# Kernel optimization log

Measured on AMD Instinct MI355X. Metric: run time of the kernel, lower is better.

## Reference

```python
import jax, jax.numpy as jnp
import numpy as np

N = 8192
D_IN, D_HID, D_OUT = 64, 128, 64


def setup_inputs() -> dict:
    key = jax.random.key(0)
    ks = jax.random.split(key, 8)
    x = jax.random.normal(ks[0], (N, D_IN), dtype=jnp.float32)
    adj = jax.random.uniform(ks[1], (N, N), dtype=jnp.float32)
    s = 0.05  # small init scale
    W0 = jax.random.normal(ks[2], (D_IN, D_HID), dtype=jnp.float32) * s
    b0 = jnp.zeros((D_HID,), dtype=jnp.float32)
    W1 = jax.random.normal(ks[3], (D_HID, D_HID), dtype=jnp.float32) * s
    b1 = jnp.zeros((D_HID,), dtype=jnp.float32)
    W2 = jax.random.normal(ks[4], (D_HID, D_OUT), dtype=jnp.float32) * s
    b2 = jnp.zeros((D_OUT,), dtype=jnp.float32)
    return {"x": x, "adj": adj, "W0": W0, "b0": b0, "W1": W1, "b1": b1, "W2": W2, "b2": b2}


def laplacian_norm(adj):
    # A_hat = A + I; D^{-1/2} A_hat D^{-1/2}
    A = adj + jnp.eye(adj.shape[0], dtype=adj.dtype)
    dinv = jax.lax.rsqrt(jnp.sum(A, axis=1))
    return A * dinv[:, None] * dinv[None, :]


def reference(x, adj, W0, b0, W1, b1, W2, b2):
    An = laplacian_norm(adj)              # [N, N], computed once, reused per layer
    h = jax.nn.relu(An @ (x @ W0) + b0)   # layer 0 + hidden act
    h = jax.nn.relu(An @ (h @ W1) + b1)   # layer 1 + hidden act
    out = An @ (h @ W2) + b2              # last layer, identity out_act
    return out
```

## Files before the change

### kernel.cpp

```cpp
#include <hip/hip_runtime.h>
#include <type_traits>

typedef unsigned short u16;
typedef unsigned int   u32;
using short8 = __attribute__((ext_vector_type(8))) short;
using f32x4  = __attribute__((ext_vector_type(4))) float;

#define GLD_AS1 const __attribute__((address_space(1))) unsigned
#define GLD_AS3 __attribute__((address_space(3))) unsigned

static constexpr int NN = 8192;

__device__ __forceinline__ u16 f2bf(float f) {
  u32 u = __builtin_bit_cast(u32, f);
  u32 r = (u + 0x7FFFu + ((u >> 16) & 1u)) >> 16;
  return (u16)r;
}
__device__ __forceinline__ float bf2f(u16 h) {
  return __builtin_bit_cast(float, (u32)h << 16);
}
__device__ __forceinline__ short8 cvt8(f32x4 f0, f32x4 f1) {
  short8 r;
#pragma unroll
  for (int i = 0; i < 4; ++i) {
    r[i]     = (short)f2bf(f0[i]);
    r[4 + i] = (short)f2bf(f1[i]);
  }
  return r;
}

__global__ __launch_bounds__(256) void rowsum_cvt_k(const float* __restrict__ adj,
                                                    u16* __restrict__ adjb,
                                                    float* __restrict__ dinv) {
  const int row = blockIdx.x;
  const f32x4* p = (const f32x4*)(adj + (size_t)row * NN);
  short8* w = (short8*)(adjb + (size_t)row * NN);
  float s = 0.f;
#pragma unroll
  for (int i = 0; i < 4; ++i) {
    const int idx = threadIdx.x + i * 256;
    f32x4 v0 = __builtin_nontemporal_load(p + 2 * idx);
    f32x4 v1 = __builtin_nontemporal_load(p + 2 * idx + 1);
    s += (v0[0] + v0[1]) + (v0[2] + v0[3]) + (v1[0] + v1[1]) + (v1[2] + v1[3]);
    w[idx] = cvt8(v0, v1);
  }
#pragma unroll
  for (int off = 32; off > 0; off >>= 1) s += __shfl_down(s, off, 64);
  __shared__ float partial[4];
  if ((threadIdx.x & 63) == 0) partial[threadIdx.x >> 6] = s;
  __syncthreads();
  if (threadIdx.x == 0)
    dinv[row] = rsqrtf(partial[0] + partial[1] + partial[2] + partial[3] + 1.0f);
}

template <typename TIN>
__global__ __launch_bounds__(256) void featmul_k(const TIN* __restrict__ X,
                                                 const float* __restrict__ W,
                                                 const float* __restrict__ dinv,
                                                 u16* __restrict__ Gt,
                                                 u16* __restrict__ U,
                                                 int K, int C) {
  __shared__ __align__(16) u16 Wt[128][128];
  __shared__ float red[4][16][32];
  const int tid = threadIdx.x;
  for (int idx = tid; idx < 128 * 128; idx += 256) {
    int c = idx & 127, k = idx >> 7;
    float w = (k < K && c < C) ? W[k * C + c] : 0.f;
    Wt[c][k] = f2bf(w);
  }
  __syncthreads();
  const int wv = tid >> 6, lane = tid & 63;
  const int q = lane >> 4, m16 = lane & 15;
  const int r0 = blockIdx.x * 16;
  const int c0 = wv * 32;
  f32x4 acc[2];
  acc[0] = {0.f, 0.f, 0.f, 0.f};
  acc[1] = {0.f, 0.f, 0.f, 0.f};
  const TIN* xrow = X + (size_t)(r0 + m16) * K;
  for (int k = 0; k < K; k += 32) {
    short8 af;
    if constexpr (std::is_same_v<TIN, float>) {
      f32x4 f0 = *(const f32x4*)(xrow + k + q * 8);
      f32x4 f1 = *(const f32x4*)(xrow + k + q * 8 + 4);
      af = cvt8(f0, f1);
    } else {
      af = __builtin_bit_cast(short8, *(const uint4*)(xrow + k + q * 8));
    }
#pragma unroll
    for (int nh = 0; nh < 2; ++nh) {
      short8 bf = *(const short8*)&Wt[c0 + nh * 16 + m16][k + q * 8];
      acc[nh] = __builtin_amdgcn_mfma_f32_16x16x32_bf16(af, bf, acc[nh], 0, 0, 0);
    }
  }
#pragma unroll
  for (int nh = 0; nh < 2; ++nh)
#pragma unroll
    for (int reg = 0; reg < 4; ++reg)
      red[wv][q * 4 + reg][nh * 16 + m16] = acc[nh][reg];
  __syncthreads();
  {
    const int cc = lane & 31, rh = lane >> 5;
    short8 t;
#pragma unroll
    for (int i = 0; i < 8; ++i) {
      int r = rh * 8 + i;
      t[i] = (short)f2bf(red[wv][r][cc] * dinv[r0 + r]);
      U[(size_t)(r0 + r) * 128 + c0 + cc] = (u16)t[i];
    }
    *(uint4*)(Gt + (size_t)(c0 + cc) * NN + r0 + rh * 8) = __builtin_bit_cast(uint4, t);
  }
}

__global__ __launch_bounds__(512, 2) void gcn_gemm(const u16* __restrict__ Adjb,
                                                   const u16* __restrict__ Gt,
                                                   float* __restrict__ P) {
  __shared__ __align__(16) u16 As[3][256 * 64];
  __shared__ __align__(16) u16 Bs[3][128 * 64];

  const int tid = threadIdx.x;
  const int wv = tid >> 6, lane = tid & 63;
  const int wm = wv >> 1, wn = wv & 1;
  const int q = lane >> 4, m16 = lane & 15;
  const int mbase = blockIdx.x * 256;
  const int kbase = blockIdx.y * 1024;
  float* Pt = P + (size_t)blockIdx.y * NN * 128;

  size_t aoff[4];
  int acl[4];
  size_t boff[2];
  int bcl[2];
#pragma unroll
  for (int i = 0; i < 4; ++i) {
    const int cl = i * 512 + tid;
    const int r = cl >> 3;
    const int g = (cl & 7) ^ (r & 7);
    aoff[i] = (size_t)(mbase + r) * NN + g * 8;
    acl[i] = cl;
  }
#pragma unroll
  for (int i = 0; i < 2; ++i) {
    const int cl = i * 512 + tid;
    const int r = cl >> 3;
    const int g = (cl & 7) ^ (r & 7);
    boff[i] = (size_t)r * NN + g * 8;
    bcl[i] = cl;
  }

  auto stage = [&](int buf, int kc) {
#pragma unroll
    for (int i = 0; i < 4; ++i)
      __builtin_amdgcn_global_load_lds((GLD_AS1*)(Adjb + aoff[i] + kc),
                                       (GLD_AS3*)(&As[buf][acl[i] * 8]), 16, 0, 0);
#pragma unroll
    for (int i = 0; i < 2; ++i)
      __builtin_amdgcn_global_load_lds((GLD_AS1*)(Gt + boff[i] + kc),
                                       (GLD_AS3*)(&Bs[buf][bcl[i] * 8]), 16, 0, 0);
  };

  f32x4 acc[4][4];
#pragma unroll
  for (int a = 0; a < 4; ++a)
#pragma unroll
    for (int b = 0; b < 4; ++b) acc[a][b] = {0.f, 0.f, 0.f, 0.f};

  stage(0, kbase);
  stage(1, kbase + 64);
  for (int t = 0; t < 16; ++t) {
    const int buf = t % 3;
    if (t < 15) {
      asm volatile("s_waitcnt vmcnt(6)" ::: "memory");
    } else {
      asm volatile("s_waitcnt vmcnt(0)" ::: "memory");
    }
    __builtin_amdgcn_s_barrier();
    asm volatile("" ::: "memory");
    if (t + 2 < 16) stage((t + 2) % 3, kbase + (t + 2) * 64);
#pragma unroll
    for (int j = 0; j < 2; ++j) {
      short8 af[4], bf[4];
#pragma unroll
      for (int i = 0; i < 4; ++i) {
        const int m = wm * 64 + i * 16 + m16;
        const int n = wn * 64 + i * 16 + m16;
        af[i] = *(const short8*)&As[buf][m * 64 + (((j * 4 + q) ^ (m & 7)) << 3)];
        bf[i] = *(const short8*)&Bs[buf][n * 64 + (((j * 4 + q) ^ (n & 7)) << 3)];
      }
#pragma unroll
      for (int a = 0; a < 4; ++a)
#pragma unroll
        for (int b = 0; b < 4; ++b)
          acc[a][b] = __builtin_amdgcn_mfma_f32_16x16x32_bf16(af[a], bf[b], acc[a][b], 0, 0, 0);
    }
  }

#pragma unroll
  for (int a = 0; a < 4; ++a) {
#pragma unroll
    for (int b = 0; b < 4; ++b) {
      const int c = wn * 64 + b * 16 + m16;
#pragma unroll
      for (int reg = 0; reg < 4; ++reg) {
        const int r = mbase + wm * 64 + a * 16 + q * 4 + reg;
        Pt[(size_t)r * 128 + c] = acc[a][b][reg];
      }
    }
  }
}

template <int RELU, int OUT_F32>
__global__ __launch_bounds__(256) void finalize_k(const float* __restrict__ P,
                                                  const u16* __restrict__ U,
                                                  const float* __restrict__ dinv,
                                                  const float* __restrict__ bias,
                                                  u16* __restrict__ Hout,
                                                  float* __restrict__ Fout) {
  const int tid = threadIdx.x;
  const int c = tid & 127;
  const int r = blockIdx.x * 2 + (tid >> 7);
  const size_t idx = (size_t)r * 128 + c;
  float s = 0.f;
#pragma unroll
  for (int k = 0; k < 8; ++k) s += P[(size_t)k * NN * 128 + idx];
  s += bf2f(U[idx]);
  s = dinv[r] * s + bias[c];
  if (RELU) s = fmaxf(s, 0.f);
  if (OUT_F32) {
    if (c < 64) Fout[(size_t)r * 64 + c] = s;
  } else {
    Hout[idx] = f2bf(s);
  }
}

extern "C" void kernel_launch(void* const* d_in, const int* in_sizes, int n_in,
                              void* d_out, int out_size, void* d_ws, size_t ws_size,
                              hipStream_t stream) {
  const float* x   = (const float*)d_in[0];
  const float* adj = (const float*)d_in[1];
  const float* W0  = (const float*)d_in[2];
  const float* b0  = (const float*)d_in[3];
  const float* W1  = (const float*)d_in[4];
  const float* b1  = (const float*)d_in[5];
  const float* W2  = (const float*)d_in[6];
  const float* b2  = (const float*)d_in[7];
  float* out = (float*)d_out;

  char* ws = (char*)d_ws;
  float* dinv = (float*)ws;
  u16* Gt     = (u16*)(ws + (1u << 20));
  u16* U      = (u16*)(ws + (4u << 20));
  u16* h      = (u16*)(ws + (6u << 20));
  float* Pp   = (float*)(ws + (8u << 20));
  u16* adjb   = (u16*)(ws + (48u << 20));

  const dim3 ggrid(32, 8);

  rowsum_cvt_k<<<NN, 256, 0, stream>>>(adj, adjb, dinv);

  featmul_k<float><<<NN / 16, 256, 0, stream>>>(x, W0, dinv, Gt, U, 64, 128);
  gcn_gemm<<<ggrid, 512, 0, stream>>>(adjb, Gt, Pp);
  finalize_k<1, 0><<<NN / 2, 256, 0, stream>>>(Pp, U, dinv, b0, h, nullptr);

  featmul_k<u16><<<NN / 16, 256, 0, stream>>>(h, W1, dinv, Gt, U, 128, 128);
  gcn_gemm<<<ggrid, 512, 0, stream>>>(adjb, Gt, Pp);
  finalize_k<1, 0><<<NN / 2, 256, 0, stream>>>(Pp, U, dinv, b1, h, nullptr);

  featmul_k<u16><<<NN / 16, 256, 0, stream>>>(h, W2, dinv, Gt, U, 128, 64);
  gcn_gemm<<<ggrid, 512, 0, stream>>>(adjb, Gt, Pp);
  finalize_k<0, 1><<<NN / 2, 256, 0, stream>>>(Pp, U, dinv, b2, nullptr, out);
}
```

Baseline: 572.8 us.

## Replace direct global-to-LDS loads with register-staged double buffering and smaller tiles

The aggregation GEMM now uses 256-thread blocks on 128x128 output tiles, so the grid doubles in the M dimension. Tiles are prefetched two steps ahead into registers and written to a double-buffered LDS after compute, replacing the triple-buffered global_load_lds path. The aim is more blocks per CU and better overlap of loads with MFMA work. In exchange it uses more registers for staging, adds explicit LDS writes, and loads the G tile twice as many times because the M tile is smaller.

```diff
diff --git a/kernel.cpp b/kernel.cpp
--- a/kernel.cpp
+++ b/kernel.cpp
@@ -5,9 +5,6 @@
 typedef unsigned int   u32;
 using short8 = __attribute__((ext_vector_type(8))) short;
 using f32x4  = __attribute__((ext_vector_type(4))) float;
-
-#define GLD_AS1 const __attribute__((address_space(1))) unsigned
-#define GLD_AS3 __attribute__((address_space(3))) unsigned
 
 static constexpr int NN = 8192;
 
@@ -111,70 +108,61 @@
   }
 }
 
-__global__ __launch_bounds__(512, 2) void gcn_gemm(const u16* __restrict__ Adjb,
+__global__ __launch_bounds__(256, 2) void gcn_gemm(const u16* __restrict__ Adjb,
                                                    const u16* __restrict__ Gt,
                                                    float* __restrict__ P) {
-  __shared__ __align__(16) u16 As[3][256 * 64];
-  __shared__ __align__(16) u16 Bs[3][128 * 64];
+  __shared__ __align__(16) u16 As[2][128 * 64];
+  __shared__ __align__(16) u16 Bs[2][128 * 64];
 
   const int tid = threadIdx.x;
   const int wv = tid >> 6, lane = tid & 63;
   const int wm = wv >> 1, wn = wv & 1;
   const int q = lane >> 4, m16 = lane & 15;
-  const int mbase = blockIdx.x * 256;
+  const int mbase = blockIdx.x * 128;
   const int kbase = blockIdx.y * 1024;
   float* Pt = P + (size_t)blockIdx.y * NN * 128;
 
-  size_t aoff[4];
-  int acl[4];
-  size_t boff[2];
-  int bcl[2];
-#pragma unroll
-  for (int i = 0; i < 4; ++i) {
-    const int cl = i * 512 + tid;
-    const int r = cl >> 3;
-    const int g = (cl & 7) ^ (r & 7);
-    aoff[i] = (size_t)(mbase + r) * NN + g * 8;
-    acl[i] = cl;
-  }
-#pragma unroll
-  for (int i = 0; i < 2; ++i) {
-    const int cl = i * 512 + tid;
-    const int r = cl >> 3;
-    const int g = (cl & 7) ^ (r & 7);
-    boff[i] = (size_t)r * NN + g * 8;
-    bcl[i] = cl;
-  }
-
-  auto stage = [&](int buf, int kc) {
-#pragma unroll
-    for (int i = 0; i < 4; ++i)
-      __builtin_amdgcn_global_load_lds((GLD_AS1*)(Adjb + aoff[i] + kc),
-                                       (GLD_AS3*)(&As[buf][acl[i] * 8]), 16, 0, 0);
-#pragma unroll
-    for (int i = 0; i < 2; ++i)
-      __builtin_amdgcn_global_load_lds((GLD_AS1*)(Gt + boff[i] + kc),
-                                       (GLD_AS3*)(&Bs[buf][bcl[i] * 8]), 16, 0, 0);
+  const int rr = tid >> 3;
+  const int g = (tid & 7) ^ (rr & 7);
+  const u16* gA = Adjb + (size_t)(mbase + rr) * NN + kbase + g * 8;
+  const u16* gB = Gt + (size_t)rr * NN + kbase + g * 8;
+  const int lo = tid * 8;
+
+  uint4 stg[2][8];
+
+  f32x4 acc[4][4];
+#pragma unroll
+  for (int a = 0; a < 4; ++a)
+#pragma unroll
+    for (int b = 0; b < 4; ++b) acc[a][b] = {0.f, 0.f, 0.f, 0.f};
+
+  auto issue = [&](int t, int s) {
+#pragma unroll
+    for (int i = 0; i < 4; ++i) {
+      stg[s][i]     = *(const uint4*)(gA + (size_t)i * 32 * NN + t * 64);
+      stg[s][4 + i] = *(const uint4*)(gB + (size_t)i * 32 * NN + t * 64);
+    }
   };
-
-  f32x4 acc[4][4];
-#pragma unroll
-  for (int a = 0; a < 4; ++a)
-#pragma unroll
-    for (int b = 0; b < 4; ++b) acc[a][b] = {0.f, 0.f, 0.f, 0.f};
-
-  stage(0, kbase);
-  stage(1, kbase + 64);
+  auto wr = [&](int s, int buf) {
+#pragma unroll
+    for (int i = 0; i < 4; ++i) {
+      *(uint4*)&As[buf][lo + i * 2048] = stg[s][i];
+      *(uint4*)&Bs[buf][lo + i * 2048] = stg[s][4 + i];
+    }
+  };
+
+  issue(0, 0);
+  issue(1, 1);
+  asm volatile("s_waitcnt vmcnt(8)" ::: "memory");
+  wr(0, 0);
+  asm volatile("s_waitcnt lgkmcnt(0)" ::: "memory");
+  __builtin_amdgcn_s_barrier();
+  asm volatile("" ::: "memory");
+
+#pragma unroll
   for (int t = 0; t < 16; ++t) {
-    const int buf = t % 3;
-    if (t < 15) {
-      asm volatile("s_waitcnt vmcnt(6)" ::: "memory");
-    } else {
-      asm volatile("s_waitcnt vmcnt(0)" ::: "memory");
-    }
-    __builtin_amdgcn_s_barrier();
-    asm volatile("" ::: "memory");
-    if (t + 2 < 16) stage((t + 2) % 3, kbase + (t + 2) * 64);
+    const int cur = t & 1;
+    if (t + 2 < 16) issue(t + 2, cur);
 #pragma unroll
     for (int j = 0; j < 2; ++j) {
       short8 af[4], bf[4];
@@ -182,14 +170,25 @@
       for (int i = 0; i < 4; ++i) {
         const int m = wm * 64 + i * 16 + m16;
         const int n = wn * 64 + i * 16 + m16;
-        af[i] = *(const short8*)&As[buf][m * 64 + (((j * 4 + q) ^ (m & 7)) << 3)];
-        bf[i] = *(const short8*)&Bs[buf][n * 64 + (((j * 4 + q) ^ (n & 7)) << 3)];
+        af[i] = *(const short8*)&As[cur][m * 64 + (((j * 4 + q) ^ (m & 7)) << 3)];
+        bf[i] = *(const short8*)&Bs[cur][n * 64 + (((j * 4 + q) ^ (n & 7)) << 3)];
       }
 #pragma unroll
       for (int a = 0; a < 4; ++a)
 #pragma unroll
         for (int b = 0; b < 4; ++b)
           acc[a][b] = __builtin_amdgcn_mfma_f32_16x16x32_bf16(af[a], bf[b], acc[a][b], 0, 0, 0);
+    }
+    if (t < 15) {
+      if (t + 2 < 16) {
+        asm volatile("s_waitcnt vmcnt(8)" ::: "memory");
+      } else {
+        asm volatile("s_waitcnt vmcnt(0)" ::: "memory");
+      }
+      wr(cur ^ 1, cur ^ 1);
+      asm volatile("s_waitcnt lgkmcnt(0)" ::: "memory");
+      __builtin_amdgcn_s_barrier();
+      asm volatile("" ::: "memory");
     }
   }
 
@@ -252,19 +251,19 @@
   float* Pp   = (float*)(ws + (8u << 20));
   u16* adjb   = (u16*)(ws + (48u << 20));
 
-  const dim3 ggrid(32, 8);
+  const dim3 ggrid(64, 8);
 
   rowsum_cvt_k<<<NN, 256, 0, stream>>>(adj, adjb, dinv);
 
   featmul_k<float><<<NN / 16, 256, 0, stream>>>(x, W0, dinv, Gt, U, 64, 128);
-  gcn_gemm<<<ggrid, 512, 0, stream>>>(adjb, Gt, Pp);
+  gcn_gemm<<<ggrid, 256, 0, stream>>>(adjb, Gt, Pp);
   finalize_k<1, 0><<<NN / 2, 256, 0, stream>>>(Pp, U, dinv, b0, h, nullptr);
 
   featmul_k<u16><<<NN / 16, 256, 0, stream>>>(h, W1, dinv, Gt, U, 128, 128);
-  gcn_gemm<<<ggrid, 512, 0, stream>>>(adjb, Gt, Pp);
+  gcn_gemm<<<ggrid, 256, 0, stream>>>(adjb, Gt, Pp);
   finalize_k<1, 0><<<NN / 2, 256, 0, stream>>>(Pp, U, dinv, b1, h, nullptr);
 
   featmul_k<u16><<<NN / 16, 256, 0, stream>>>(h, W2, dinv, Gt, U, 128, 64);
-  gcn_gemm<<<ggrid, 512, 0, stream>>>(adjb, Gt, Pp);
+  gcn_gemm<<<ggrid, 256, 0, stream>>>(adjb, Gt, Pp);
   finalize_k<0, 1><<<NN / 2, 256, 0, stream>>>(Pp, U, dinv, b2, nullptr, out);
 }
```

Result: slower. 736.7 us (+28.6%).
